# Optimization experiments

Measured on AMD Instinct MI355X. Metric: run time of the kernel, lower is better.

The kernel has to match this reference:

```python
import jax, jax.numpy as jnp
import numpy as np

CUTOFF = 10.0
MAX_NEIGHBORS = 32
N_NODES = 8192
N_GRAPHS = 256


def setup_inputs() -> dict:
    key = jax.random.key(0)
    k1, k2 = jax.random.split(key)
    pos = jax.random.normal(k1, (N_NODES, 3), dtype=jnp.float32) * 3.0
    batch = jnp.sort(jax.random.randint(k2, (N_NODES,), 0, N_GRAPHS)).astype(jnp.int64)
    return {"pos": pos, "batch": batch}


def reference(pos, batch):
    """Radius-graph (fixed-size, padded) + gathered edge-distance norm.

    Faithful to tgnn.radius_graph semantics: for each node, up to
    MAX_NEIGHBORS neighbors within CUTOFF in the same graph, no self-loops.
    Returns (edge_index [2, N*K], edge_weight [N*K], edge_mask [N*K]);
    padded slots point to the node itself with weight 0 and mask False.
    """
    n = pos.shape[0]
    k = MAX_NEIGHBORS
    # Pairwise squared distances via Gram trick (avoids [N,N,3] intermediate).
    sq = jnp.sum(pos * pos, axis=-1)                       # [N]
    d2 = sq[:, None] + sq[None, :] - 2.0 * (pos @ pos.T)   # [N,N]
    d2 = jnp.maximum(d2, 0.0)
    same_graph = batch[:, None] == batch[None, :]
    idx = jnp.arange(n)
    not_self = idx[:, None] != idx[None, :]
    valid = same_graph & not_self & (d2 <= CUTOFF * CUTOFF)
    # Keep the k NEAREST valid neighbors per node (deterministic cap).
    neg = jnp.where(valid, -d2, -jnp.inf)
    top_vals, top_idx = jax.lax.top_k(neg, k)              # [N,k]
    edge_mask = jnp.isfinite(top_vals)                     # [N,k]
    row = jnp.broadcast_to(idx[:, None], (n, k))           # center node
    col = jnp.where(edge_mask, top_idx, row)               # neighbor (safe pad)
    row = row.reshape(-1)
    col = col.reshape(-1)
    mask = edge_mask.reshape(-1)
    diff = pos[row] - pos[col]                             # [N*k, 3]
    d2e = jnp.sum(diff * diff, axis=-1)
    edge_weight = jnp.sqrt(jnp.where(mask, d2e, 1.0)) * mask.astype(pos.dtype)
    edge_index = jnp.stack([row, col], axis=0)             # [2, N*k]
    return edge_index, edge_weight, mask
```

## Files before the change

kernel.cpp:

```cpp
#include <hip/hip_runtime.h>
#include <stdint.h>


constexpr int   N_NODES = 8192;
constexpr int   K       = 32;
constexpr int   NK      = N_NODES * K;
constexpr float CUT2    = 100.0f;
constexpr int   CMAX    = 4;

__device__ __forceinline__ unsigned long long umin64(unsigned long long a,
                                                     unsigned long long b) {
    return a < b ? a : b;
}

__device__ __forceinline__ unsigned long long shfl_xor_u64(unsigned long long v,
                                                           int mask) {
    int lo = (int)(unsigned int)v;
    int hi = (int)(unsigned int)(v >> 32);
    lo = __shfl_xor(lo, mask, 64);
    hi = __shfl_xor(hi, mask, 64);
    return ((unsigned long long)(unsigned int)hi << 32) | (unsigned int)lo;
}

__device__ __forceinline__ unsigned score_key(
        const float* __restrict__ pos, int j, int i,
        float xi, float yi, float zi, float sqi, bool active) {
    unsigned key = 0xFFFFFFFFu;
    if (active) {
        const float xj = pos[3 * j], yj = pos[3 * j + 1], zj = pos[3 * j + 2];
        const float sqj = __fadd_rn(__fadd_rn(__fmul_rn(xj, xj), __fmul_rn(yj, yj)),
                                    __fmul_rn(zj, zj));
        const float dot = __fadd_rn(__fadd_rn(__fmul_rn(xi, xj), __fmul_rn(yi, yj)),
                                    __fmul_rn(zi, zj));
        float d2 = __fsub_rn(__fadd_rn(sqi, sqj), __fmul_rn(2.0f, dot));
        d2 = fmaxf(d2, 0.0f);
        if (d2 <= CUT2)
            key = (__float_as_uint(d2) & ~0x1FFFu) | (unsigned)j;
    }
    return key;
}

__global__ __launch_bounds__(256) void radius_graph_kernel(
        const float* __restrict__ pos,
        const int*   __restrict__ batch,
        float* __restrict__ out) {
    const int gid  = blockIdx.x * 256 + threadIdx.x;
    const int i    = gid >> 6;
    const int lane = threadIdx.x & 63;
    if (i >= N_NODES) return;

    const int b = batch[i];

    const int idxL = i - 64 + lane;
    const int idxR = i + lane;
    const int wL = batch[max(idxL, 0)];
    const int wR = batch[min(idxR, N_NODES - 1)];
    const unsigned long long m1 = __ballot(idxL >= 0 && wL == b);
    const unsigned long long m2 = __ballot(idxR < N_NODES && wR == b);

    int s, e;
    if ((m1 & 1ull) || (~m2 == 0ull)) {
        int lo = 0, hi = i;
        while (lo < hi) { int mid = (lo + hi) >> 1; if (batch[mid] <  b) lo = mid + 1; else hi = mid; }
        s = lo;
        lo = i + 1; hi = N_NODES;
        while (lo < hi) { int mid = (lo + hi) >> 1; if (batch[mid] <= b) lo = mid + 1; else hi = mid; }
        e = lo;
    } else {
        s = m1 ? (i - 64 + __ffsll((long long)m1) - 1) : i;
        e = i + __ffsll((long long)(~m2)) - 1;
    }

    const float xi = pos[3 * i], yi = pos[3 * i + 1], zi = pos[3 * i + 2];
    const float sqi = __fadd_rn(__fadd_rn(__fmul_rn(xi, xi), __fmul_rn(yi, yi)),
                                __fmul_rn(zi, zi));

    const int ncand = e - s - 1;
    unsigned slotKey = 0xFFFFFFFFu;

    if (ncand <= 32) {
        const int jc = s + lane + ((s + lane >= i) ? 1 : 0);
        unsigned key = score_key(pos, jc, i, xi, yi, zi, sqi, lane < ncand);
#pragma unroll
        for (int k = 2; k <= 32; k <<= 1) {
#pragma unroll
            for (int jj = k >> 1; jj > 0; jj >>= 1) {
                const unsigned partner = (unsigned)__shfl_xor((int)key, jj, 64);
                const bool up    = ((lane & k) == 0);
                const bool lower = ((lane & jj) == 0);
                const unsigned mn = min(key, partner);
                const unsigned mx = max(key, partner);
                key = ((lower == up) ? mn : mx);
            }
        }
        slotKey = key;
    } else if (e - s <= 64) {
        const int j = s + lane;
        unsigned key = score_key(pos, j, i, xi, yi, zi, sqi, j < e && j != i);
#pragma unroll
        for (int k = 2; k <= 64; k <<= 1) {
#pragma unroll
            for (int jj = k >> 1; jj > 0; jj >>= 1) {
                const unsigned partner = (unsigned)__shfl_xor((int)key, jj, 64);
                const bool up    = ((lane & k) == 0);
                const bool lower = ((lane & jj) == 0);
                const unsigned mn = min(key, partner);
                const unsigned mx = max(key, partner);
                key = ((lower == up) ? mn : mx);
            }
        }
        slotKey = key;
    } else {
        unsigned long long key[CMAX];
#pragma unroll
        for (int c = 0; c < CMAX; ++c) {
            const int j = s + lane + 64 * c;
            unsigned long long kk = ~0ULL;
            if (j < e && j != i) {
                const float xj = pos[3 * j], yj = pos[3 * j + 1], zj = pos[3 * j + 2];
                const float sqj = __fadd_rn(__fadd_rn(__fmul_rn(xj, xj), __fmul_rn(yj, yj)),
                                            __fmul_rn(zj, zj));
                const float dot = __fadd_rn(__fadd_rn(__fmul_rn(xi, xj), __fmul_rn(yi, yj)),
                                            __fmul_rn(zi, zj));
                float d2 = __fsub_rn(__fadd_rn(sqi, sqj), __fmul_rn(2.0f, dot));
                d2 = fmaxf(d2, 0.0f);
                if (d2 <= CUT2)
                    kk = (((unsigned long long)__float_as_uint(d2)) << 32) | (unsigned int)j;
            }
            key[c] = kk;
        }
        unsigned long long res = ~0ULL;
        for (int t = 0; t < K; ++t) {
            unsigned long long m = key[0];
#pragma unroll
            for (int c = 1; c < CMAX; ++c) m = umin64(m, key[c]);
#pragma unroll
            for (int off = 1; off < 64; off <<= 1)
                m = umin64(m, shfl_xor_u64(m, off));
            if (lane == t) res = m;
#pragma unroll
            for (int c = 0; c < CMAX; ++c) if (key[c] == m) key[c] = ~0ULL;
        }
        if (res != ~0ULL)
            slotKey = ((unsigned)(res >> 32) & ~0x1FFFu) | (unsigned)(res & 0x1FFFu);
    }

    const int      slot  = lane & (K - 1);
    const unsigned kS    = (unsigned)__shfl((int)slotKey, slot, 64);
    const bool     valid = (kS != 0xFFFFFFFFu);
    const int      col   = valid ? (int)(kS & 0x1FFFu) : i;
    const int      o     = i * K + slot;

    if (lane < K) {
        out[o]      = (float)i;
        out[NK + o] = (float)col;
    } else {
        float w = 0.0f;
        if (valid) {
            const float dx = __fsub_rn(xi, pos[3 * col]);
            const float dy = __fsub_rn(yi, pos[3 * col + 1]);
            const float dz = __fsub_rn(zi, pos[3 * col + 2]);
            const float d2e = __fadd_rn(__fadd_rn(__fmul_rn(dx, dx), __fmul_rn(dy, dy)),
                                        __fmul_rn(dz, dz));
            w = __fsqrt_rn(d2e);
        }
        out[2 * NK + o] = w;
        out[3 * NK + o] = valid ? 1.0f : 0.0f;
    }
}

extern "C" void kernel_launch(void* const* d_in, const int* in_sizes, int n_in,
                              void* d_out, int out_size, void* d_ws, size_t ws_size,
                              hipStream_t stream) {
    const float* pos   = (const float*)d_in[0];
    const int*   batch = (const int*)d_in[1];
    float*       out   = (float*)d_out;

    radius_graph_kernel<<<(N_NODES * 64) / 256, 256, 0, stream>>>(pos, batch, out);
}
```

Before: 59.18 us.

## Process two nodes per wavefront using 32-lane half-waves

Each 64-lane wavefront now handles two nodes, one per 32-lane half, which halves the thread count and the grid size. Graph-boundary detection, candidate scoring and the bitonic or iterative top-k all operate per half-wave. Branch selection is made uniform across the wavefront with ballots, and a new two-register bitonic path covers 33 to 64 candidates. Every lane now writes all four outputs for its slot instead of splitting row/col and weight/mask across lanes. The aim is less idle lane work in the common small-graph case, at the cost of both halves running the costlier path whenever either one needs it.

```diff
diff --git a/kernel.cpp b/kernel.cpp
--- a/kernel.cpp
+++ b/kernel.cpp
@@ -44,31 +44,46 @@
         const float* __restrict__ pos,
         const int*   __restrict__ batch,
         float* __restrict__ out) {
-    const int gid  = blockIdx.x * 256 + threadIdx.x;
-    const int i    = gid >> 6;
-    const int lane = threadIdx.x & 63;
-    if (i >= N_NODES) return;
+    const int tid = threadIdx.x;
+    const int gid = blockIdx.x * 256 + tid;
+    const int i   = gid >> 5;
+    const int l   = tid & 31;
+    const int h   = (tid >> 5) & 1;
 
     const int b = batch[i];
 
-    const int idxL = i - 64 + lane;
-    const int idxR = i + lane;
+    const int idxL = i - 32 + l;
+    const int idxR = i + l;
     const int wL = batch[max(idxL, 0)];
     const int wR = batch[min(idxR, N_NODES - 1)];
-    const unsigned long long m1 = __ballot(idxL >= 0 && wL == b);
-    const unsigned long long m2 = __ballot(idxR < N_NODES && wR == b);
+    const unsigned m1 = (unsigned)(__ballot(idxL >= 0 && wL == b) >> (h * 32));
+    const unsigned m2 = (unsigned)(__ballot(idxR < N_NODES && wR == b) >> (h * 32));
 
     int s, e;
-    if ((m1 & 1ull) || (~m2 == 0ull)) {
-        int lo = 0, hi = i;
-        while (lo < hi) { int mid = (lo + hi) >> 1; if (batch[mid] <  b) lo = mid + 1; else hi = mid; }
-        s = lo;
-        lo = i + 1; hi = N_NODES;
-        while (lo < hi) { int mid = (lo + hi) >> 1; if (batch[mid] <= b) lo = mid + 1; else hi = mid; }
-        e = lo;
+    const bool ext = ((m1 & 1u) != 0) || (~m2 == 0u);
+    if (__ballot(ext)) {
+        const int idxL2 = i - 64 + l;
+        const int idxR2 = i + 32 + l;
+        const int wL2 = batch[max(idxL2, 0)];
+        const int wR2 = batch[min(idxR2, N_NODES - 1)];
+        const unsigned mL2 = (unsigned)(__ballot(idxL2 >= 0 && wL2 == b) >> (h * 32));
+        const unsigned mR2 = (unsigned)(__ballot(idxR2 < N_NODES && wR2 == b) >> (h * 32));
+        const unsigned long long M1 = ((unsigned long long)m1 << 32) | mL2;
+        const unsigned long long M2 = ((unsigned long long)mR2 << 32) | m2;
+        if ((M1 & 1ull) || (~M2 == 0ull)) {
+            int lo = 0, hi = i;
+            while (lo < hi) { int mid = (lo + hi) >> 1; if (batch[mid] <  b) lo = mid + 1; else hi = mid; }
+            s = lo;
+            lo = i + 1; hi = N_NODES;
+            while (lo < hi) { int mid = (lo + hi) >> 1; if (batch[mid] <= b) lo = mid + 1; else hi = mid; }
+            e = lo;
+        } else {
+            s = M1 ? (i - 64 + __ffsll((long long)M1) - 1) : i;
+            e = i + __ffsll((long long)~M2) - 1;
+        }
     } else {
-        s = m1 ? (i - 64 + __ffsll((long long)m1) - 1) : i;
-        e = i + __ffsll((long long)(~m2)) - 1;
+        s = m1 ? (i - 32 + __ffs((int)m1) - 1) : i;
+        e = i + __ffs((int)~m2) - 1;
     }
 
     const float xi = pos[3 * i], yi = pos[3 * i + 1], zi = pos[3 * i + 2];
@@ -76,45 +91,13 @@
                                 __fmul_rn(zi, zi));
 
     const int ncand = e - s - 1;
-    unsigned slotKey = 0xFFFFFFFFu;
+    unsigned slotKey;
 
-    if (ncand <= 32) {
-        const int jc = s + lane + ((s + lane >= i) ? 1 : 0);
-        unsigned key = score_key(pos, jc, i, xi, yi, zi, sqi, lane < ncand);
-#pragma unroll
-        for (int k = 2; k <= 32; k <<= 1) {
-#pragma unroll
-            for (int jj = k >> 1; jj > 0; jj >>= 1) {
-                const unsigned partner = (unsigned)__shfl_xor((int)key, jj, 64);
-                const bool up    = ((lane & k) == 0);
-                const bool lower = ((lane & jj) == 0);
-                const unsigned mn = min(key, partner);
-                const unsigned mx = max(key, partner);
-                key = ((lower == up) ? mn : mx);
-            }
-        }
-        slotKey = key;
-    } else if (e - s <= 64) {
-        const int j = s + lane;
-        unsigned key = score_key(pos, j, i, xi, yi, zi, sqi, j < e && j != i);
-#pragma unroll
-        for (int k = 2; k <= 64; k <<= 1) {
-#pragma unroll
-            for (int jj = k >> 1; jj > 0; jj >>= 1) {
-                const unsigned partner = (unsigned)__shfl_xor((int)key, jj, 64);
-                const bool up    = ((lane & k) == 0);
-                const bool lower = ((lane & jj) == 0);
-                const unsigned mn = min(key, partner);
-                const unsigned mx = max(key, partner);
-                key = ((lower == up) ? mn : mx);
-            }
-        }
-        slotKey = key;
-    } else {
+    if (__ballot(e - s > 64)) {
         unsigned long long key[CMAX];
 #pragma unroll
         for (int c = 0; c < CMAX; ++c) {
-            const int j = s + lane + 64 * c;
+            const int j = s + l + 32 * c;
             unsigned long long kk = ~0ULL;
             if (j < e && j != i) {
                 const float xj = pos[3 * j], yj = pos[3 * j + 1], zj = pos[3 * j + 2];
@@ -135,38 +118,72 @@
 #pragma unroll
             for (int c = 1; c < CMAX; ++c) m = umin64(m, key[c]);
 #pragma unroll
-            for (int off = 1; off < 64; off <<= 1)
+            for (int off = 1; off < 32; off <<= 1)
                 m = umin64(m, shfl_xor_u64(m, off));
-            if (lane == t) res = m;
+            if (l == t) res = m;
 #pragma unroll
             for (int c = 0; c < CMAX; ++c) if (key[c] == m) key[c] = ~0ULL;
         }
-        if (res != ~0ULL)
-            slotKey = ((unsigned)(res >> 32) & ~0x1FFFu) | (unsigned)(res & 0x1FFFu);
+        slotKey = (res != ~0ULL)
+                ? (((unsigned)(res >> 32) & ~0x1FFFu) | (unsigned)(res & 0x1FFFu))
+                : 0xFFFFFFFFu;
+    } else if (__ballot(ncand > 32)) {
+        const int j0 = s + l, j1 = s + 32 + l;
+        unsigned k0 = score_key(pos, j0, i, xi, yi, zi, sqi, j0 < e && j0 != i);
+        unsigned k1 = score_key(pos, j1, i, xi, yi, zi, sqi, j1 < e && j1 != i);
+#pragma unroll
+        for (int k = 2; k <= 64; k <<= 1) {
+#pragma unroll
+            for (int jj = k >> 1; jj > 0; jj >>= 1) {
+                if (jj >= 32) {
+                    const unsigned mn = min(k0, k1);
+                    const unsigned mx = max(k0, k1);
+                    k0 = mn; k1 = mx;
+                } else {
+                    const unsigned p0 = (unsigned)__shfl_xor((int)k0, jj, 64);
+                    const unsigned p1 = (unsigned)__shfl_xor((int)k1, jj, 64);
+                    const bool lower = ((l & jj) == 0);
+                    const bool up0 = ((l & k) == 0);
+                    const bool up1 = (((32 + l) & k) == 0);
+                    k0 = (lower == up0) ? min(k0, p0) : max(k0, p0);
+                    k1 = (lower == up1) ? min(k1, p1) : max(k1, p1);
+                }
+            }
+        }
+        slotKey = k0;
+    } else {
+        const int jc = s + l + ((s + l >= i) ? 1 : 0);
+        unsigned key = score_key(pos, jc, i, xi, yi, zi, sqi, l < ncand);
+#pragma unroll
+        for (int k = 2; k <= 32; k <<= 1) {
+#pragma unroll
+            for (int jj = k >> 1; jj > 0; jj >>= 1) {
+                const unsigned partner = (unsigned)__shfl_xor((int)key, jj, 64);
+                const bool up    = ((l & k) == 0);
+                const bool lower = ((l & jj) == 0);
+                key = (lower == up) ? min(key, partner) : max(key, partner);
+            }
+        }
+        slotKey = key;
     }
 
-    const int      slot  = lane & (K - 1);
-    const unsigned kS    = (unsigned)__shfl((int)slotKey, slot, 64);
-    const bool     valid = (kS != 0xFFFFFFFFu);
-    const int      col   = valid ? (int)(kS & 0x1FFFu) : i;
-    const int      o     = i * K + slot;
+    const bool valid = (slotKey != 0xFFFFFFFFu);
+    const int  col   = valid ? (int)(slotKey & 0x1FFFu) : i;
+    const int  o     = i * K + l;
 
-    if (lane < K) {
-        out[o]      = (float)i;
-        out[NK + o] = (float)col;
-    } else {
-        float w = 0.0f;
-        if (valid) {
-            const float dx = __fsub_rn(xi, pos[3 * col]);
-            const float dy = __fsub_rn(yi, pos[3 * col + 1]);
-            const float dz = __fsub_rn(zi, pos[3 * col + 2]);
-            const float d2e = __fadd_rn(__fadd_rn(__fmul_rn(dx, dx), __fmul_rn(dy, dy)),
-                                        __fmul_rn(dz, dz));
-            w = __fsqrt_rn(d2e);
-        }
-        out[2 * NK + o] = w;
-        out[3 * NK + o] = valid ? 1.0f : 0.0f;
+    out[o]      = (float)i;
+    out[NK + o] = (float)col;
+    float w = 0.0f;
+    if (valid) {
+        const float dx = __fsub_rn(xi, pos[3 * col]);
+        const float dy = __fsub_rn(yi, pos[3 * col + 1]);
+        const float dz = __fsub_rn(zi, pos[3 * col + 2]);
+        const float d2e = __fadd_rn(__fadd_rn(__fmul_rn(dx, dx), __fmul_rn(dy, dy)),
+                                    __fmul_rn(dz, dz));
+        w = __fsqrt_rn(d2e);
     }
+    out[2 * NK + o] = w;
+    out[3 * NK + o] = valid ? 1.0f : 0.0f;
 }
 
 extern "C" void kernel_launch(void* const* d_in, const int* in_sizes, int n_in,
@@ -176,5 +193,5 @@
     const int*   batch = (const int*)d_in[1];
     float*       out   = (float*)d_out;
 
-    radius_graph_kernel<<<(N_NODES * 64) / 256, 256, 0, stream>>>(pos, batch, out);
+    radius_graph_kernel<<<(N_NODES * 32) / 256, 256, 0, stream>>>(pos, batch, out);
 }
```

New measurement: 58.46 us. About the same (-1.2%).
